# Performance work log

Measured on AMD Instinct MI355X. Metric: run time of the kernel, lower is better.

Reference implementation:

```python
import jax, jax.numpy as jnp
from jax import lax
import numpy as np

INPUT_DIM, STATE_DIM, CONV_K, EXPAND = 1024, 16, 4, 2
INNER = INPUT_DIM * EXPAND
BATCH, SEQ = 2, 2048


def setup_inputs() -> dict:
    key = jax.random.key(0)
    ks = jax.random.split(key, 6)
    x = jax.random.normal(ks[0], (BATCH, SEQ, INPUT_DIM), jnp.float32)
    W_in = jax.random.normal(ks[1], (2 * INNER, INPUT_DIM), jnp.float32) * 0.02
    conv_w = jax.random.normal(ks[2], (INNER, 1, CONV_K), jnp.float32) * 0.1  # depthwise (O, I/g=1, K)
    conv_b = jnp.zeros((INNER,), jnp.float32)
    A_log = jax.random.normal(ks[3], (INNER, STATE_DIM), jnp.float32)
    D = jnp.ones((INNER,), jnp.float32)
    W_out = jax.random.normal(ks[4], (INPUT_DIM, INNER), jnp.float32) * 0.02
    return {"x": x, "W_in": W_in, "conv_w": conv_w, "conv_b": conv_b,
            "A_log": A_log, "D": D, "W_out": W_out}


def reference(x, W_in, conv_w, conv_b, A_log, D, W_out):
    b, s, _ = x.shape
    inner = W_in.shape[0] // 2
    K = conv_w.shape[-1]
    state = A_log.shape[1]

    xr = x @ W_in.T                              # (b, s, 2*inner)
    x_ssm, res = xr[..., :inner], xr[..., inner:]

    # Causal depthwise conv: torch pads K-1 both sides then truncates to seq -> left-pad K-1, VALID conv.
    xc = jnp.transpose(x_ssm, (0, 2, 1))         # (b, inner, s)
    xc = jnp.pad(xc, ((0, 0), (0, 0), (K - 1, 0)))
    xc = lax.conv_general_dilated(xc, conv_w, (1,), 'VALID',
                                  feature_group_count=inner,
                                  dimension_numbers=('NCH', 'OIH', 'NCH'))
    x_conv = jax.nn.silu(jnp.transpose(xc, (0, 2, 1)) + conv_b)   # (b, s, inner)

    delta = jax.nn.softplus(x_conv)              # (b, s, inner)
    A = -jnp.exp(A_log)                          # (inner, state)
    A_d = jnp.exp(delta[..., None] * A)          # (b, s, inner, state)
    Bx = x_conv * x_conv                         # B_t * x_t (B = x = x_conv in this module)

    def step(h, inp):
        a_t, bx_t, c_t = inp                     # (b,inner,state), (b,inner), (b,inner)
        h = a_t * h + bx_t[..., None]
        y = c_t * jnp.sum(h, axis=-1)            # reduce over state -> (b, inner)
        return h, y

    h0 = jnp.zeros((b, inner, state), x.dtype)
    _, ys = lax.scan(step, h0, (jnp.moveaxis(A_d, 1, 0),
                                jnp.moveaxis(Bx, 1, 0),
                                jnp.moveaxis(x_conv, 1, 0)))
    y_ssm = jnp.moveaxis(ys, 0, 1)               # (b, s, inner)

    y = y_ssm * jax.nn.silu(res) + D * x_conv
    return y @ W_out.T                           # (b, s, input_dim)
```

## Files before the change

### kernel.cpp

```cpp
#include <hip/hip_runtime.h>
#include <hip/hip_bf16.h>
#include <math.h>

#define INPUT_DIM 1024
#define STATE_DIM 16
#define CONV_KK   4
#define INNER     2048
#define BATCH     2
#define SEQ       2048
#define M_TOT     (BATCH*SEQ)
#define N1        (2*INNER)
#define K1        INPUT_DIM
#define N2        INPUT_DIM
#define K2        INNER
#define NCHUNK    64
#define CLEN      (SEQ/NCHUNK)

typedef __attribute__((ext_vector_type(8))) short short8;
typedef __attribute__((ext_vector_type(4))) float f32x4;
typedef unsigned short ushort;

__device__ __forceinline__ float fast_softplus(float x) {
    return x > 20.f ? x : __logf(1.f + __expf(x));
}
__device__ __forceinline__ float fast_silu(float x) {
    return x * __builtin_amdgcn_rcpf(1.f + __expf(-x));
}
__device__ __forceinline__ ushort f2bf(float f) {
    unsigned u = __float_as_uint(f);
    u = (u + 0x7FFF + ((u >> 16) & 1)) >> 16;
    return (ushort)u;
}

__global__ __launch_bounds__(256) void cvt_bf16_kernel(
        const float* __restrict__ in, ushort* __restrict__ out, int n8)
{
    int i = blockIdx.x * 256 + threadIdx.x;
    if (i >= n8) return;
    const float4* p = (const float4*)in + (size_t)i * 2;
    float4 v0 = p[0], v1 = p[1];
    ushort u[8] = { f2bf(v0.x), f2bf(v0.y), f2bf(v0.z), f2bf(v0.w),
                    f2bf(v1.x), f2bf(v1.y), f2bf(v1.z), f2bf(v1.w) };
    *(short8*)(out + (size_t)i * 8) = *(short8*)u;
}

template<int BM, int BN, int WROWS, int WCOLS>
__global__ __launch_bounds__(256) void gemm_bf16_nt(
        const ushort* __restrict__ A, const ushort* __restrict__ B,
        float* __restrict__ C, int M, int N, int K)
{
    constexpr int MR = BM / WROWS / 16;
    constexpr int NR = BN / WCOLS / 16;
    __shared__ ushort As[BM][32];
    __shared__ ushort Bs[BN][32];

    const int tid  = threadIdx.x;
    const int w    = tid >> 6;
    const int lane = tid & 63;
    const int bm   = blockIdx.y * BM;
    const int bn   = blockIdx.x * BN;
    const int wm0  = (w / WCOLS) * (BM / WROWS);
    const int wn0  = (w % WCOLS) * (BN / WCOLS);

    const int srow = lane >> 2;
    const int scol = (lane & 3) * 8;

    f32x4 acc[MR][NR] = {};

    for (int k0 = 0; k0 < K; k0 += 32) {
        __syncthreads();
#pragma unroll
        for (int r0 = w * 16; r0 < BM; r0 += 64) {
            const ushort* ga = A + (size_t)(bm + r0 + srow) * K + k0 + scol;
            __builtin_amdgcn_global_load_lds(
                (const __attribute__((address_space(1))) void*)ga,
                (__attribute__((address_space(3))) void*)&As[r0][0], 16, 0, 0);
        }
#pragma unroll
        for (int r0 = w * 16; r0 < BN; r0 += 64) {
            const ushort* gb = B + (size_t)(bn + r0 + srow) * K + k0 + scol;
            __builtin_amdgcn_global_load_lds(
                (const __attribute__((address_space(1))) void*)gb,
                (__attribute__((address_space(3))) void*)&Bs[r0][0], 16, 0, 0);
        }
        __syncthreads();

        short8 a[MR], b[NR];
#pragma unroll
        for (int i = 0; i < MR; i++)
            a[i] = *(const short8*)&As[wm0 + i * 16 + (lane & 15)][(lane >> 4) * 8];
#pragma unroll
        for (int j = 0; j < NR; j++)
            b[j] = *(const short8*)&Bs[wn0 + j * 16 + (lane & 15)][(lane >> 4) * 8];
#pragma unroll
        for (int i = 0; i < MR; i++)
#pragma unroll
            for (int j = 0; j < NR; j++)
                acc[i][j] = __builtin_amdgcn_mfma_f32_16x16x32_bf16(
                    a[i], b[j], acc[i][j], 0, 0, 0);
    }

#pragma unroll
    for (int i = 0; i < MR; i++)
#pragma unroll
        for (int j = 0; j < NR; j++)
#pragma unroll
            for (int r = 0; r < 4; r++) {
                int row = bm + wm0 + i * 16 + (lane >> 4) * 4 + r;
                int col = bn + wn0 + j * 16 + (lane & 15);
                C[(size_t)row * N + col] = acc[i][j][r];
            }
}

__global__ __launch_bounds__(256) void scan_stats_fused(
        const float* __restrict__ xr,
        const float* __restrict__ conv_w,
        const float* __restrict__ conv_b,
        const float* __restrict__ A_log,
        float* __restrict__ Hc,
        float* __restrict__ Dsum)
{
    const int gid = blockIdx.x * 256 + threadIdx.x;
    const int c     = gid & (INNER - 1);
    const int chunk = (gid >> 11) & (NCHUNK - 1);
    const int b     = gid >> 17;

    const float4 w4  = *(const float4*)(conv_w + c * 4);
    const float bias = conv_b[c];

    float negA[16];
    {
        const float4* ap = (const float4*)(A_log + c * 16);
#pragma unroll
        for (int q = 0; q < 4; q++) {
            float4 v = ap[q];
            negA[q*4+0] = -__expf(v.x); negA[q*4+1] = -__expf(v.y);
            negA[q*4+2] = -__expf(v.z); negA[q*4+3] = -__expf(v.w);
        }
    }

    const int s0 = chunk * CLEN;
    const float* xp = xr + ((size_t)(b * SEQ + s0)) * N1 + c;

    float xm1 = 0.f, xm2 = 0.f, xm3 = 0.f;
    if (s0 > 0) { xm1 = xp[-N1]; xm2 = xp[-2*N1]; xm3 = xp[-3*N1]; }

    float h[16] = {};
    float dsum = 0.f;
    for (int s = 0; s < CLEN; s++) {
        float x0  = xp[(size_t)s * N1];
        float acc = bias + w4.x*xm3 + w4.y*xm2 + w4.z*xm1 + w4.w*x0;
        xm3 = xm2; xm2 = xm1; xm1 = x0;
        float xc    = fast_silu(acc);
        float delta = fast_softplus(xc);
        dsum += delta;
        float bx = xc * xc;
#pragma unroll
        for (int st = 0; st < 16; st++)
            h[st] = __expf(delta * negA[st]) * h[st] + bx;
    }

    const size_t cb = (size_t)b * NCHUNK + chunk;
#pragma unroll
    for (int st = 0; st < 16; st++)
        Hc[(cb * 16 + st) * INNER + c] = h[st];
    Dsum[cb * INNER + c] = dsum;
}

__global__ __launch_bounds__(256) void scan_carry(
        float* __restrict__ Hc,
        const float* __restrict__ Dsum,
        const float* __restrict__ A_log)
{
    const int tid = blockIdx.x * 256 + threadIdx.x;
    const int c  = tid & (INNER - 1);
    const int st = (tid >> 11) & 15;
    const int b  = tid >> 15;

    const float negA = -__expf(A_log[c * STATE_DIM + st]);
    float carry = 0.f;
    for (int j = 0; j < NCHUNK; j++) {
        const size_t cb  = (size_t)b * NCHUNK + j;
        const size_t idx = (cb * 16 + st) * INNER + c;
        float hend = Hc[idx];
        float P    = __expf(Dsum[cb * INNER + c] * negA);
        Hc[idx] = carry;
        carry = P * carry + hend;
    }
}

__global__ __launch_bounds__(256) void scan_apply_fused(
        const float* __restrict__ xr,
        const float* __restrict__ conv_w,
        const float* __restrict__ conv_b,
        const float* __restrict__ A_log,
        const float* __restrict__ Dv,
        const float* __restrict__ Hc,
        ushort* __restrict__ y_bf)
{
    const int gid = blockIdx.x * 256 + threadIdx.x;
    const int c     = gid & (INNER - 1);
    const int chunk = (gid >> 11) & (NCHUNK - 1);
    const int b     = gid >> 17;

    const float4 w4  = *(const float4*)(conv_w + c * 4);
    const float bias = conv_b[c];
    const float Dc   = Dv[c];

    float negA[16];
    {
        const float4* ap = (const float4*)(A_log + c * 16);
#pragma unroll
        for (int q = 0; q < 4; q++) {
            float4 v = ap[q];
            negA[q*4+0] = -__expf(v.x); negA[q*4+1] = -__expf(v.y);
            negA[q*4+2] = -__expf(v.z); negA[q*4+3] = -__expf(v.w);
        }
    }

    const int s0 = chunk * CLEN;
    const size_t row0 = (size_t)(b * SEQ + s0);
    const float* xp = xr + row0 * N1 + c;
    const float* rp = xr + row0 * N1 + INNER + c;
    ushort*      yp = y_bf + row0 * INNER + c;

    float xm1 = 0.f, xm2 = 0.f, xm3 = 0.f;
    if (s0 > 0) { xm1 = xp[-N1]; xm2 = xp[-2*N1]; xm3 = xp[-3*N1]; }

    const size_t cb = (size_t)b * NCHUNK + chunk;
    float h[16];
#pragma unroll
    for (int st = 0; st < 16; st++)
        h[st] = Hc[(cb * 16 + st) * INNER + c];

    for (int s = 0; s < CLEN; s++) {
        float x0  = xp[(size_t)s * N1];
        float acc = bias + w4.x*xm3 + w4.y*xm2 + w4.z*xm1 + w4.w*x0;
        xm3 = xm2; xm2 = xm1; xm1 = x0;
        float xc    = fast_silu(acc);
        float delta = fast_softplus(xc);
        float bx    = xc * xc;
#pragma unroll
        for (int st = 0; st < 16; st++)
            h[st] = __expf(delta * negA[st]) * h[st] + bx;

        float s01 = (h[0]+h[1]) + (h[2]+h[3]);
        float s23 = (h[4]+h[5]) + (h[6]+h[7]);
        float s45 = (h[8]+h[9]) + (h[10]+h[11]);
        float s67 = (h[12]+h[13]) + (h[14]+h[15]);
        float sum = (s01 + s23) + (s45 + s67);

        float r = rp[(size_t)s * N1];
        float y = xc * sum * fast_silu(r) + Dc * xc;
        yp[(size_t)s * INNER] = f2bf(y);
    }
}

extern "C" void kernel_launch(void* const* d_in, const int* in_sizes, int n_in,
                              void* d_out, int out_size, void* d_ws, size_t ws_size,
                              hipStream_t stream)
{
    const float* x      = (const float*)d_in[0];
    const float* W_in   = (const float*)d_in[1];
    const float* conv_w = (const float*)d_in[2];
    const float* conv_b = (const float*)d_in[3];
    const float* A_log  = (const float*)d_in[4];
    const float* Dv     = (const float*)d_in[5];
    const float* W_out  = (const float*)d_in[6];
    float* out = (float*)d_out;

    char* ws = (char*)d_ws;
    float*  xr      = (float*)ws;   ws += (size_t)M_TOT * N1 * 4;
    float*  Hc      = (float*)ws;   ws += (size_t)BATCH * NCHUNK * STATE_DIM * INNER * 4;
    float*  Dsum    = (float*)ws;   ws += (size_t)BATCH * NCHUNK * INNER * 4;
    ushort* x_bf    = (ushort*)ws;  ws += (size_t)M_TOT * K1 * 2;
    ushort* Win_bf  = (ushort*)ws;  ws += (size_t)N1 * K1 * 2;
    ushort* Wout_bf = (ushort*)ws;  ws += (size_t)N2 * K2 * 2;
    ushort* y_bf    = (ushort*)ws;  ws += (size_t)M_TOT * INNER * 2;

    cvt_bf16_kernel<<<(M_TOT * K1 / 8) / 256, 256, 0, stream>>>(x, x_bf, M_TOT * K1 / 8);
    cvt_bf16_kernel<<<(N1 * K1 / 8) / 256, 256, 0, stream>>>(W_in, Win_bf, N1 * K1 / 8);
    cvt_bf16_kernel<<<(N2 * K2 / 8) / 256, 256, 0, stream>>>(W_out, Wout_bf, N2 * K2 / 8);

    gemm_bf16_nt<128,128,2,2><<<dim3(N1/128, M_TOT/128), 256, 0, stream>>>(
        x_bf, Win_bf, xr, M_TOT, N1, K1);

    scan_stats_fused<<<(BATCH * NCHUNK * INNER) / 256, 256, 0, stream>>>(
        xr, conv_w, conv_b, A_log, Hc, Dsum);
    scan_carry<<<(BATCH * STATE_DIM * INNER) / 256, 256, 0, stream>>>(
        Hc, Dsum, A_log);
    scan_apply_fused<<<(BATCH * NCHUNK * INNER) / 256, 256, 0, stream>>>(
        xr, conv_w, conv_b, A_log, Dv, Hc, y_bf);

    gemm_bf16_nt<128,64,2,2><<<dim3(N2/64, M_TOT/128), 256, 0, stream>>>(
        y_bf, Wout_bf, out, M_TOT, N2, K2);
}
```

Before: 258.4 us.

## Deepen GEMM K-tile to 64 with XOR-swizzled LDS and fuse bf16 conversions

The GEMM K-step grows from 32 to 64, halving the number of barrier-separated load/compute iterations. LDS columns are XOR-swizzled by row so that MFMA fragment reads avoid bank conflicts. The three fp32-to-bf16 conversion launches are merged into one kernel that picks its source by index range. The cost is double the LDS per block, which may lower occupancy.

Measured after the change: 250.7 us. -3.0%, faster.

```diff
diff --git a/kernel.cpp b/kernel.cpp
--- a/kernel.cpp
+++ b/kernel.cpp
@@ -32,16 +32,23 @@
     return (ushort)u;
 }
 
-__global__ __launch_bounds__(256) void cvt_bf16_kernel(
-        const float* __restrict__ in, ushort* __restrict__ out, int n8)
-{
+__global__ __launch_bounds__(256) void cvt_bf16_fused(
+        const float* __restrict__ x,   ushort* __restrict__ x_bf,
+        const float* __restrict__ wi,  ushort* __restrict__ wi_bf,
+        const float* __restrict__ wo,  ushort* __restrict__ wo_bf)
+{
+    const int NA = M_TOT * K1 / 8;
+    const int NB = N1 * K1 / 8;
     int i = blockIdx.x * 256 + threadIdx.x;
-    if (i >= n8) return;
-    const float4* p = (const float4*)in + (size_t)i * 2;
+    const float* in; ushort* out; int idx;
+    if (i < NA)            { in = x;  out = x_bf;  idx = i; }
+    else if (i < NA + NB)  { in = wi; out = wi_bf; idx = i - NA; }
+    else                   { in = wo; out = wo_bf; idx = i - NA - NB; }
+    const float4* p = (const float4*)in + (size_t)idx * 2;
     float4 v0 = p[0], v1 = p[1];
     ushort u[8] = { f2bf(v0.x), f2bf(v0.y), f2bf(v0.z), f2bf(v0.w),
                     f2bf(v1.x), f2bf(v1.y), f2bf(v1.z), f2bf(v1.w) };
-    *(short8*)(out + (size_t)i * 8) = *(short8*)u;
+    *(short8*)(out + (size_t)idx * 8) = *(short8*)u;
 }
 
 template<int BM, int BN, int WROWS, int WCOLS>
@@ -51,8 +58,8 @@
 {
     constexpr int MR = BM / WROWS / 16;
     constexpr int NR = BN / WCOLS / 16;
-    __shared__ ushort As[BM][32];
-    __shared__ ushort Bs[BN][32];
+    __shared__ ushort As[BM][64];
+    __shared__ ushort Bs[BN][64];
 
     const int tid  = threadIdx.x;
     const int w    = tid >> 6;
@@ -62,42 +69,48 @@
     const int wm0  = (w / WCOLS) * (BM / WROWS);
     const int wn0  = (w % WCOLS) * (BN / WCOLS);
 
-    const int srow = lane >> 2;
-    const int scol = (lane & 3) * 8;
+    const int srow  = lane >> 3;
+    const int sslot = (lane & 7) ^ srow;
+    const int scol  = sslot * 8;
 
     f32x4 acc[MR][NR] = {};
 
-    for (int k0 = 0; k0 < K; k0 += 32) {
+    for (int k0 = 0; k0 < K; k0 += 64) {
         __syncthreads();
 #pragma unroll
-        for (int r0 = w * 16; r0 < BM; r0 += 64) {
-            const ushort* ga = A + (size_t)(bm + r0 + srow) * K + k0 + scol;
+        for (int j8 = w; j8 < BM / 8; j8 += 4) {
+            const ushort* ga = A + (size_t)(bm + j8 * 8 + srow) * K + k0 + scol;
             __builtin_amdgcn_global_load_lds(
                 (const __attribute__((address_space(1))) void*)ga,
-                (__attribute__((address_space(3))) void*)&As[r0][0], 16, 0, 0);
-        }
-#pragma unroll
-        for (int r0 = w * 16; r0 < BN; r0 += 64) {
-            const ushort* gb = B + (size_t)(bn + r0 + srow) * K + k0 + scol;
+                (__attribute__((address_space(3))) void*)&As[j8 * 8][0], 16, 0, 0);
+        }
+#pragma unroll
+        for (int j8 = w; j8 < BN / 8; j8 += 4) {
+            const ushort* gb = B + (size_t)(bn + j8 * 8 + srow) * K + k0 + scol;
             __builtin_amdgcn_global_load_lds(
                 (const __attribute__((address_space(1))) void*)gb,
-                (__attribute__((address_space(3))) void*)&Bs[r0][0], 16, 0, 0);
+                (__attribute__((address_space(3))) void*)&Bs[j8 * 8][0], 16, 0, 0);
         }
         __syncthreads();
 
-        short8 a[MR], b[NR];
-#pragma unroll
-        for (int i = 0; i < MR; i++)
-            a[i] = *(const short8*)&As[wm0 + i * 16 + (lane & 15)][(lane >> 4) * 8];
-#pragma unroll
-        for (int j = 0; j < NR; j++)
-            b[j] = *(const short8*)&Bs[wn0 + j * 16 + (lane & 15)][(lane >> 4) * 8];
-#pragma unroll
-        for (int i = 0; i < MR; i++)
+#pragma unroll
+        for (int ks = 0; ks < 2; ks++) {
+            const int lslot = ks * 4 + (lane >> 4);
+            const int pcol  = (lslot ^ (lane & 7)) * 8;
+            short8 a[MR], b[NR];
+#pragma unroll
+            for (int i = 0; i < MR; i++)
+                a[i] = *(const short8*)&As[wm0 + i * 16 + (lane & 15)][pcol];
 #pragma unroll
             for (int j = 0; j < NR; j++)
-                acc[i][j] = __builtin_amdgcn_mfma_f32_16x16x32_bf16(
-                    a[i], b[j], acc[i][j], 0, 0, 0);
+                b[j] = *(const short8*)&Bs[wn0 + j * 16 + (lane & 15)][pcol];
+#pragma unroll
+            for (int i = 0; i < MR; i++)
+#pragma unroll
+                for (int j = 0; j < NR; j++)
+                    acc[i][j] = __builtin_amdgcn_mfma_f32_16x16x32_bf16(
+                        a[i], b[j], acc[i][j], 0, 0, 0);
+        }
     }
 
 #pragma unroll
@@ -278,9 +291,11 @@
     ushort* Wout_bf = (ushort*)ws;  ws += (size_t)N2 * K2 * 2;
     ushort* y_bf    = (ushort*)ws;  ws += (size_t)M_TOT * INNER * 2;
 
-    cvt_bf16_kernel<<<(M_TOT * K1 / 8) / 256, 256, 0, stream>>>(x, x_bf, M_TOT * K1 / 8);
-    cvt_bf16_kernel<<<(N1 * K1 / 8) / 256, 256, 0, stream>>>(W_in, Win_bf, N1 * K1 / 8);
-    cvt_bf16_kernel<<<(N2 * K2 / 8) / 256, 256, 0, stream>>>(W_out, Wout_bf, N2 * K2 / 8);
+    {
+        const int total8 = (M_TOT * K1 + N1 * K1 + N2 * K2) / 8;
+        cvt_bf16_fused<<<total8 / 256, 256, 0, stream>>>(
+            x, x_bf, W_in, Win_bf, W_out, Wout_bf);
+    }
 
     gemm_bf16_nt<128,128,2,2><<<dim3(N1/128, M_TOT/128), 256, 0, stream>>>(
         x_bf, Win_bf, xr, M_TOT, N1, K1);
```
